# Optimization experiments

Measured on AMD Instinct MI355X. Metric: run time of the kernel, lower is better.

The kernel has to match this reference:

```python
import jax, jax.numpy as jnp
import numpy as np

N_VERTEX = 16384
D_IN = 64
HIDDEN = 64
D_OUT = 8
N_REGIONS = 64


def setup_inputs() -> dict:
    key = jax.random.key(0)
    ks = jax.random.split(key, 16)
    h = jax.random.normal(ks[0], (N_VERTEX, D_IN), dtype=jnp.float32)
    norm_adj = jax.random.uniform(ks[1], (N_VERTEX, N_VERTEX), dtype=jnp.float32) / N_VERTEX
    region_index = jax.random.randint(ks[2], (N_VERTEX,), 0, N_REGIONS, dtype=jnp.int32)
    s = 1.0 / np.sqrt(D_IN)
    W1 = jax.random.normal(ks[3], (D_IN, HIDDEN), dtype=jnp.float32) * s
    L1 = jax.random.normal(ks[4], (D_IN, HIDDEN), dtype=jnp.float32) * s
    rw1 = jax.random.normal(ks[5], (N_REGIONS, HIDDEN), dtype=jnp.float32) * 0.1 + 1.0
    rb1 = jax.random.normal(ks[6], (N_REGIONS, HIDDEN), dtype=jnp.float32) * 0.1
    sh = 1.0 / np.sqrt(HIDDEN)
    W2 = jax.random.normal(ks[7], (HIDDEN, HIDDEN), dtype=jnp.float32) * sh
    L2 = jax.random.normal(ks[8], (HIDDEN, HIDDEN), dtype=jnp.float32) * sh
    rw2 = jax.random.normal(ks[9], (N_REGIONS, HIDDEN), dtype=jnp.float32) * 0.1 + 1.0
    rb2 = jax.random.normal(ks[10], (N_REGIONS, HIDDEN), dtype=jnp.float32) * 0.1
    Wout = jax.random.normal(ks[11], (D_OUT, HIDDEN), dtype=jnp.float32) * sh
    bout = jax.random.normal(ks[12], (D_OUT,), dtype=jnp.float32) * 0.1
    return dict(h=h, norm_adj=norm_adj, region_index=region_index,
                W1=W1, L1=L1, rw1=rw1, rb1=rb1,
                W2=W2, L2=L2, rw2=rw2, rb2=rb2,
                Wout=Wout, bout=bout)


def _reg_conv(h, norm_adj, region_index, W, L, reg_w, reg_b):
    # ra = h @ W ; rb = norm_adj @ (h @ L)   [N, d_out]
    z = h @ W + norm_adj @ (h @ L)
    # per-vertex region gather of affine params (the irregular-access hot path)
    return z * reg_w[region_index] + reg_b[region_index]


def reference(h, norm_adj, region_index, W1, L1, rw1, rb1, W2, L2, rw2, rb2, Wout, bout):
    x = jax.nn.relu(_reg_conv(h, norm_adj, region_index, W1, L1, rw1, rb1))
    x = jax.nn.relu(_reg_conv(x, norm_adj, region_index, W2, L2, rw2, rb2))
    return x @ Wout.T + bout  # [N, d_out]
```

## Files before the change

kernel.cpp:

```cpp
#include <hip/hip_runtime.h>
#include <stdint.h>

#define NV 16384
#define DH 64
#define BTS (NV + 64)
#define BTQS (NV + 64)
#define BK 256
#define LDST 264
#define LDST8 272
#define NCH 32
#define SCUP 16384.0f
#define SCDN 6.103515625e-05f

typedef __attribute__((ext_vector_type(4))) float f32x4;
typedef __attribute__((ext_vector_type(8))) short s16x8;

static __device__ __forceinline__ unsigned short f2bf(float f) {
  union { float f; unsigned u; } x; x.f = f;
  unsigned r = x.u + 0x7fffu + ((x.u >> 16) & 1u);
  return (unsigned short)(r >> 16);
}

static __device__ __forceinline__ s16x8 cvt8(f32x4 a, f32x4 b) {
  s16x8 r;
  r[0] = (short)f2bf(a[0]); r[1] = (short)f2bf(a[1]);
  r[2] = (short)f2bf(a[2]); r[3] = (short)f2bf(a[3]);
  r[4] = (short)f2bf(b[0]); r[5] = (short)f2bf(b[1]);
  r[6] = (short)f2bf(b[2]); r[7] = (short)f2bf(b[3]);
  return r;
}

__global__ __launch_bounds__(256) void k_prep(
    const float* __restrict__ h, const float* __restrict__ W1,
    const float* __restrict__ L1, float* __restrict__ Z,
    unsigned short* __restrict__ Bt) {
  __shared__ float Ws[4096], Ls[4096], hs[16 * 64];
  int tid = threadIdx.x;
  for (int i = tid; i < 4096; i += 256) { Ws[i] = W1[i]; Ls[i] = L1[i]; }
  int r = tid >> 6, c = tid & 63;
  int i0 = blockIdx.x << 4;
  #pragma unroll
  for (int m = 0; m < 4; ++m)
    hs[(r + 4 * m) * 64 + c] = h[(size_t)(i0 + r + 4 * m) * 64 + c];
  __syncthreads();
  float a1[4] = {0.f, 0.f, 0.f, 0.f};
  float a2[4] = {0.f, 0.f, 0.f, 0.f};
  #pragma unroll 8
  for (int k = 0; k < 64; ++k) {
    float wv = Ws[k * 64 + c];
    float lv = Ls[k * 64 + c];
    #pragma unroll
    for (int m = 0; m < 4; ++m) {
      float hv = hs[(r + 4 * m) * 64 + k];
      a1[m] += hv * wv;
      a2[m] += hv * lv;
    }
  }
  #pragma unroll
  for (int m = 0; m < 4; ++m) {
    int i = i0 + r + 4 * m;
    Z[(size_t)i * 64 + c] = a1[m];
    Bt[(size_t)c * BTS + i] = f2bf(a2[m]);
  }
}

__global__ __launch_bounds__(256, 2) void k_adj(
    const float* __restrict__ adj, const unsigned short* __restrict__ Bt,
    float* __restrict__ P, unsigned char* __restrict__ adj8) {
  __shared__ __align__(16) unsigned short Blds[2 * 64 * LDST];
  const int tid = threadIdx.x;
  const int lane = tid & 63;
  const int w = tid >> 6;
  const int l15 = lane & 15;
  const int kgrp = lane >> 4;
  const int xb = blockIdx.x;
  const int yb = blockIdx.y;
  const int row = (xb << 6) + (w << 4) + l15;
  const int kbase = yb << 13;

  const int srow = tid >> 4;
  const int sc16 = tid & 15;
  const unsigned short* sbase = Bt + (size_t)srow * BTS + kbase + sc16 * 8;
  unsigned short* lbase = Blds + srow * LDST + sc16 * 8;

  const float* ap = adj + (size_t)row * NV + kbase + kgrp * 8;
  unsigned char* a8w = adj8 +
      ((((size_t)xb * 2 + yb) * 4 + w) * 256) * 512 + (size_t)lane * 8;
  const int bofs0 = (l15 +  0) * LDST + kgrp * 8;
  const int bofs1 = (l15 + 16) * LDST + kgrp * 8;
  const int bofs2 = (l15 + 32) * LDST + kgrp * 8;
  const int bofs3 = (l15 + 48) * LDST + kgrp * 8;

  f32x4 sr0, sr1, sr2, sr3, sr4, sr5, sr6, sr7;
#define STAGE_LOAD(KC)                                                   \
  { const unsigned short* s_ = sbase + (KC);                             \
    sr0 = *(const f32x4*)(s_);                                           \
    sr1 = *(const f32x4*)(s_ + 128);                                     \
    sr2 = *(const f32x4*)(s_ + (size_t)16 * BTS);                        \
    sr3 = *(const f32x4*)(s_ + (size_t)16 * BTS + 128);                  \
    sr4 = *(const f32x4*)(s_ + (size_t)32 * BTS);                        \
    sr5 = *(const f32x4*)(s_ + (size_t)32 * BTS + 128);                  \
    sr6 = *(const f32x4*)(s_ + (size_t)48 * BTS);                        \
    sr7 = *(const f32x4*)(s_ + (size_t)48 * BTS + 128); }
#define STAGE_WRITE(BUF)                                                 \
  { unsigned short* d_ = lbase + (BUF) * (64 * LDST);                    \
    *(f32x4*)(d_) = sr0;                                                 \
    *(f32x4*)(d_ + 128) = sr1;                                           \
    *(f32x4*)(d_ + 16 * LDST) = sr2;                                     \
    *(f32x4*)(d_ + 16 * LDST + 128) = sr3;                               \
    *(f32x4*)(d_ + 32 * LDST) = sr4;                                     \
    *(f32x4*)(d_ + 32 * LDST + 128) = sr5;                               \
    *(f32x4*)(d_ + 48 * LDST) = sr6;                                     \
    *(f32x4*)(d_ + 48 * LDST + 128) = sr7; }

  f32x4 aj0a, aj0b, aj1a, aj1b, aj2a, aj2b, aj3a, aj3b;

  STAGE_LOAD(0);
  aj0a = *(const f32x4*)(ap +   0); aj0b = *(const f32x4*)(ap +   4);
  aj1a = *(const f32x4*)(ap +  32); aj1b = *(const f32x4*)(ap +  36);
  aj2a = *(const f32x4*)(ap +  64); aj2b = *(const f32x4*)(ap +  68);
  aj3a = *(const f32x4*)(ap +  96); aj3b = *(const f32x4*)(ap + 100);
  STAGE_WRITE(0);
  __syncthreads();

  f32x4 acc0 = {0.f, 0.f, 0.f, 0.f};
  f32x4 acc1 = {0.f, 0.f, 0.f, 0.f};
  f32x4 acc2 = {0.f, 0.f, 0.f, 0.f};
  f32x4 acc3 = {0.f, 0.f, 0.f, 0.f};

#define ITER(II, AJA, AJB)                                               \
  {                                                                      \
    s16x8 af = cvt8(AJA, AJB);                                           \
    unsigned pk0 = __builtin_amdgcn_cvt_pk_fp8_f32(AJA[0] * SCUP, AJA[1] * SCUP, 0, false); \
    pk0 = __builtin_amdgcn_cvt_pk_fp8_f32(AJA[2] * SCUP, AJA[3] * SCUP, pk0, true);         \
    unsigned pk1 = __builtin_amdgcn_cvt_pk_fp8_f32(AJB[0] * SCUP, AJB[1] * SCUP, 0, false); \
    pk1 = __builtin_amdgcn_cvt_pk_fp8_f32(AJB[2] * SCUP, AJB[3] * SCUP, pk1, true);         \
    *(unsigned long long*)(a8w + (size_t)((t << 3) + (II)) * 512) =      \
        (unsigned long long)pk0 | ((unsigned long long)pk1 << 32);       \
    int ci = ((t << 3) + (II) + 4) & 255;                                \
    AJA = *(const f32x4*)(ap + (size_t)ci * 32);                         \
    AJB = *(const f32x4*)(ap + (size_t)ci * 32 + 4);                     \
    s16x8 cb0 = *(const s16x8*)(bb + bofs0 + (II) * 32);                 \
    s16x8 cb1 = *(const s16x8*)(bb + bofs1 + (II) * 32);                 \
    s16x8 cb2 = *(const s16x8*)(bb + bofs2 + (II) * 32);                 \
    s16x8 cb3 = *(const s16x8*)(bb + bofs3 + (II) * 32);                 \
    acc0 = __builtin_amdgcn_mfma_f32_16x16x32_bf16(af, cb0, acc0, 0, 0, 0); \
    acc1 = __builtin_amdgcn_mfma_f32_16x16x32_bf16(af, cb1, acc1, 0, 0, 0); \
    acc2 = __builtin_amdgcn_mfma_f32_16x16x32_bf16(af, cb2, acc2, 0, 0, 0); \
    acc3 = __builtin_amdgcn_mfma_f32_16x16x32_bf16(af, cb3, acc3, 0, 0, 0); \
  }

  for (int t = 0; t < NCH; ++t) {
    const unsigned short* bb = Blds + (t & 1) * (64 * LDST);
    if (t + 1 < NCH) STAGE_LOAD((t + 1) * BK);
    ITER(0, aj0a, aj0b)
    ITER(1, aj1a, aj1b)
    ITER(2, aj2a, aj2b)
    ITER(3, aj3a, aj3b)
    ITER(4, aj0a, aj0b)
    ITER(5, aj1a, aj1b)
    ITER(6, aj2a, aj2b)
    ITER(7, aj3a, aj3b)
    if (t + 1 < NCH) STAGE_WRITE((t + 1) & 1);
    __syncthreads();
  }

  int zr = (xb << 6) + (w << 4) + (kgrp << 2);
  float* pp = P + (size_t)yb * NV * 64 + (size_t)zr * 64 + l15;
  #pragma unroll
  for (int r = 0; r < 4; ++r) {
    pp[(size_t)r * 64 +  0] = acc0[r];
    pp[(size_t)r * 64 + 16] = acc1[r];
    pp[(size_t)r * 64 + 32] = acc2[r];
    pp[(size_t)r * 64 + 48] = acc3[r];
  }
#undef STAGE_LOAD
#undef STAGE_WRITE
#undef ITER
}

__global__ __launch_bounds__(256, 2) void k_adj8(
    const unsigned char* __restrict__ adj8, const unsigned char* __restrict__ Btq,
    float* __restrict__ P) {
  __shared__ __align__(16) unsigned char Blds[2 * 64 * LDST8];
  const int tid = threadIdx.x;
  const int lane = tid & 63;
  const int w = tid >> 6;
  const int l15 = lane & 15;
  const int kgrp = lane >> 4;
  const int xb = blockIdx.x;
  const int yb = blockIdx.y;
  const int kbase = yb << 13;

  const int srow = tid >> 4;
  const int sc16 = tid & 15;
  const unsigned char* sbase = Btq + (size_t)srow * BTQS + kbase + sc16 * 16;
  unsigned char* lbase = Blds + srow * LDST8 + sc16 * 16;

  const unsigned char* ap8 = adj8 +
      ((((size_t)xb * 2 + yb) * 4 + w) * 256) * 512 + (size_t)lane * 8;
  const int bofs0 = (l15 +  0) * LDST8 + kgrp * 8;
  const int bofs1 = (l15 + 16) * LDST8 + kgrp * 8;
  const int bofs2 = (l15 + 32) * LDST8 + kgrp * 8;
  const int bofs3 = (l15 + 48) * LDST8 + kgrp * 8;

  f32x4 sr0, sr1, sr2, sr3;
#define STAGE_LOAD8(KC)                                                  \
  { const unsigned char* s_ = sbase + (KC);                              \
    sr0 = *(const f32x4*)(s_);                                           \
    sr1 = *(const f32x4*)(s_ + (size_t)16 * BTQS);                       \
    sr2 = *(const f32x4*)(s_ + (size_t)32 * BTQS);                       \
    sr3 = *(const f32x4*)(s_ + (size_t)48 * BTQS); }
#define STAGE_WRITE8(BUF)                                                \
  { unsigned char* d_ = lbase + (BUF) * (64 * LDST8);                    \
    *(f32x4*)(d_) = sr0;                                                 \
    *(f32x4*)(d_ + 16 * LDST8) = sr1;                                    \
    *(f32x4*)(d_ + 32 * LDST8) = sr2;                                    \
    *(f32x4*)(d_ + 48 * LDST8) = sr3; }

  unsigned long long aj0, aj1, aj2, aj3;

  STAGE_LOAD8(0);
  aj0 = *(const unsigned long long*)(ap8 +    0);
  aj1 = *(const unsigned long long*)(ap8 +  512);
  aj2 = *(const unsigned long long*)(ap8 + 1024);
  aj3 = *(const unsigned long long*)(ap8 + 1536);
  STAGE_WRITE8(0);
  __syncthreads();

  f32x4 acc0 = {0.f, 0.f, 0.f, 0.f};
  f32x4 acc1 = {0.f, 0.f, 0.f, 0.f};
  f32x4 acc2 = {0.f, 0.f, 0.f, 0.f};
  f32x4 acc3 = {0.f, 0.f, 0.f, 0.f};

#define ITER8(II, AJ)                                                    \
  {                                                                      \
    long long a_ = (long long)AJ;                                        \
    int ci = ((t << 3) + (II) + 4) & 255;                                \
    AJ = *(const unsigned long long*)(ap8 + (size_t)ci * 512);           \
    long long b0 = *(const long long*)(bb + bofs0 + (II) * 32);          \
    long long b1 = *(const long long*)(bb + bofs1 + (II) * 32);          \
    long long b2 = *(const long long*)(bb + bofs2 + (II) * 32);          \
    long long b3 = *(const long long*)(bb + bofs3 + (II) * 32);          \
    acc0 = __builtin_amdgcn_mfma_f32_16x16x32_fp8_fp8(a_, b0, acc0, 0, 0, 0); \
    acc1 = __builtin_amdgcn_mfma_f32_16x16x32_fp8_fp8(a_, b1, acc1, 0, 0, 0); \
    acc2 = __builtin_amdgcn_mfma_f32_16x16x32_fp8_fp8(a_, b2, acc2, 0, 0, 0); \
    acc3 = __builtin_amdgcn_mfma_f32_16x16x32_fp8_fp8(a_, b3, acc3, 0, 0, 0); \
  }

  for (int t = 0; t < NCH; ++t) {
    const unsigned char* bb = Blds + (t & 1) * (64 * LDST8);
    if (t + 1 < NCH) STAGE_LOAD8((t + 1) * BK);
    ITER8(0, aj0)
    ITER8(1, aj1)
    ITER8(2, aj2)
    ITER8(3, aj3)
    ITER8(4, aj0)
    ITER8(5, aj1)
    ITER8(6, aj2)
    ITER8(7, aj3)
    if (t + 1 < NCH) STAGE_WRITE8((t + 1) & 1);
    __syncthreads();
  }

  int zr = (xb << 6) + (w << 4) + (kgrp << 2);
  float* pp = P + (size_t)yb * NV * 64 + (size_t)zr * 64 + l15;
  #pragma unroll
  for (int r = 0; r < 4; ++r) {
    pp[(size_t)r * 64 +  0] = acc0[r] * SCDN;
    pp[(size_t)r * 64 + 16] = acc1[r] * SCDN;
    pp[(size_t)r * 64 + 32] = acc2[r] * SCDN;
    pp[(size_t)r * 64 + 48] = acc3[r] * SCDN;
  }
#undef STAGE_LOAD8
#undef STAGE_WRITE8
#undef ITER8
}

__global__ __launch_bounds__(256) void k_mid(
    float* __restrict__ Z, const float* __restrict__ P,
    const int* __restrict__ reg,
    const float* __restrict__ rw1, const float* __restrict__ rb1,
    const float* __restrict__ W2, const float* __restrict__ L2,
    unsigned char* __restrict__ Btq) {
  __shared__ float Ws[4096], Ls[4096], xs[16 * 64];
  int tid = threadIdx.x;
  for (int i = tid; i < 4096; i += 256) { Ws[i] = W2[i]; Ls[i] = L2[i]; }
  int r = tid >> 6, c = tid & 63;
  int i0 = blockIdx.x << 4;
  #pragma unroll
  for (int m = 0; m < 4; ++m) {
    int i = i0 + r + 4 * m;
    int ri = reg[i];
    size_t o = (size_t)i * 64 + c;
    float z = Z[o] + P[o] + P[(size_t)NV * 64 + o];
    float x = z * rw1[ri * 64 + c] + rb1[ri * 64 + c];
    xs[(r + 4 * m) * 64 + c] = fmaxf(x, 0.f);
  }
  __syncthreads();
  float a1[4] = {0.f, 0.f, 0.f, 0.f};
  float a2[4] = {0.f, 0.f, 0.f, 0.f};
  #pragma unroll 8
  for (int k = 0; k < 64; ++k) {
    float wv = Ws[k * 64 + c];
    float lv = Ls[k * 64 + c];
    #pragma unroll
    for (int m = 0; m < 4; ++m) {
      float xv = xs[(r + 4 * m) * 64 + k];
      a1[m] += xv * wv;
      a2[m] += xv * lv;
    }
  }
  #pragma unroll
  for (int m = 0; m < 4; ++m) {
    int i = i0 + r + 4 * m;
    Z[(size_t)i * 64 + c] = a1[m];
    unsigned q = __builtin_amdgcn_cvt_pk_fp8_f32(a2[m], 0.0f, 0, false);
    Btq[(size_t)c * BTQS + i] = (unsigned char)(q & 0xff);
  }
}

__global__ __launch_bounds__(256) void k_out(
    const float* __restrict__ Z, const float* __restrict__ P,
    const int* __restrict__ reg,
    const float* __restrict__ rw2, const float* __restrict__ rb2,
    const float* __restrict__ Wout, const float* __restrict__ bout,
    float* __restrict__ out) {
  __shared__ float xs[16 * 64];
  int tid = threadIdx.x;
  int r = tid >> 6, c = tid & 63;
  int i0 = blockIdx.x << 4;
  #pragma unroll
  for (int m = 0; m < 4; ++m) {
    int i = i0 + r + 4 * m;
    int ri = reg[i];
    size_t o = (size_t)i * 64 + c;
    float z = Z[o] + P[o] + P[(size_t)NV * 64 + o];
    float x = z * rw2[ri * 64 + c] + rb2[ri * 64 + c];
    xs[(r + 4 * m) * 64 + c] = fmaxf(x, 0.f);
  }
  __syncthreads();
  if (c < 8) {
    #pragma unroll
    for (int m = 0; m < 4; ++m) {
      int i = i0 + r + 4 * m;
      float a = bout[c];
      #pragma unroll 8
      for (int k = 0; k < 64; ++k) a += xs[(r + 4 * m) * 64 + k] * Wout[c * 64 + k];
      out[(size_t)i * 8 + c] = a;
    }
  }
}

extern "C" void kernel_launch(void* const* d_in, const int* in_sizes, int n_in,
                              void* d_out, int out_size, void* d_ws, size_t ws_size,
                              hipStream_t stream) {
  const float* h    = (const float*)d_in[0];
  const float* adj  = (const float*)d_in[1];
  const int*   reg  = (const int*)d_in[2];
  const float* W1   = (const float*)d_in[3];
  const float* L1   = (const float*)d_in[4];
  const float* rw1  = (const float*)d_in[5];
  const float* rb1  = (const float*)d_in[6];
  const float* W2   = (const float*)d_in[7];
  const float* L2   = (const float*)d_in[8];
  const float* rw2  = (const float*)d_in[9];
  const float* rb2  = (const float*)d_in[10];
  const float* Wout = (const float*)d_in[11];
  const float* bout = (const float*)d_in[12];
  float* out = (float*)d_out;

  char* ws = (char*)d_ws;
  float* Z            = (float*)(ws);
  unsigned short* Bt  = (unsigned short*)(ws + ((size_t)4  << 20));
  float* P            = (float*)(ws + ((size_t)8  << 20));
  unsigned char* Btq  = (unsigned char*)(ws + ((size_t)16 << 20));
  unsigned char* adj8 = (unsigned char*)(ws + ((size_t)20 << 20));

  k_prep<<<NV / 16, 256, 0, stream>>>(h, W1, L1, Z, Bt);
  k_adj<<<dim3(NV / 64, 2), 256, 0, stream>>>(adj, Bt, P, adj8);
  k_mid<<<NV / 16, 256, 0, stream>>>(Z, P, reg, rw1, rb1, W2, L2, Btq);
  k_adj8<<<dim3(NV / 64, 2), 256, 0, stream>>>(adj8, Btq, P);
  k_out<<<NV / 16, 256, 0, stream>>>(Z, P, reg, rw2, rb2, Wout, bout, out);
}
```

Baseline: 405.6 us.

## Use FP8 MFMA for first adjacency pass and split K four ways

The first adjacency GEMM now quantizes both the adjacency rows and the h@L1 operand to FP8 and uses the FP8 16x16x32 MFMA, replacing the bf16 path. This removes the bf16 conversion work and halves the shared-memory staging. The K dimension is also split into four partial sums instead of two, doubling the grid and raising occupancy hints to 4 blocks per CU, with the consumers now summing four partial planes. This trades accuracy for speed, since the first layer's operand also becomes FP8, and it adds extra partial-sum memory traffic.

```diff
diff --git a/kernel.cpp b/kernel.cpp
--- a/kernel.cpp
+++ b/kernel.cpp
@@ -2,38 +2,19 @@
 #include <stdint.h>
 
 #define NV 16384
-#define DH 64
-#define BTS (NV + 64)
 #define BTQS (NV + 64)
 #define BK 256
-#define LDST 264
 #define LDST8 272
-#define NCH 32
+#define NCH 16
 #define SCUP 16384.0f
 #define SCDN 6.103515625e-05f
 
 typedef __attribute__((ext_vector_type(4))) float f32x4;
-typedef __attribute__((ext_vector_type(8))) short s16x8;
-
-static __device__ __forceinline__ unsigned short f2bf(float f) {
-  union { float f; unsigned u; } x; x.f = f;
-  unsigned r = x.u + 0x7fffu + ((x.u >> 16) & 1u);
-  return (unsigned short)(r >> 16);
-}
-
-static __device__ __forceinline__ s16x8 cvt8(f32x4 a, f32x4 b) {
-  s16x8 r;
-  r[0] = (short)f2bf(a[0]); r[1] = (short)f2bf(a[1]);
-  r[2] = (short)f2bf(a[2]); r[3] = (short)f2bf(a[3]);
-  r[4] = (short)f2bf(b[0]); r[5] = (short)f2bf(b[1]);
-  r[6] = (short)f2bf(b[2]); r[7] = (short)f2bf(b[3]);
-  return r;
-}
 
 __global__ __launch_bounds__(256) void k_prep(
     const float* __restrict__ h, const float* __restrict__ W1,
     const float* __restrict__ L1, float* __restrict__ Z,
-    unsigned short* __restrict__ Bt) {
+    unsigned char* __restrict__ Btq1) {
   __shared__ float Ws[4096], Ls[4096], hs[16 * 64];
   int tid = threadIdx.x;
   for (int i = tid; i < 4096; i += 256) { Ws[i] = W1[i]; Ls[i] = L1[i]; }
@@ -60,14 +41,15 @@
   for (int m = 0; m < 4; ++m) {
     int i = i0 + r + 4 * m;
     Z[(size_t)i * 64 + c] = a1[m];
-    Bt[(size_t)c * BTS + i] = f2bf(a2[m]);
-  }
-}
-
-__global__ __launch_bounds__(256, 2) void k_adj(
-    const float* __restrict__ adj, const unsigned short* __restrict__ Bt,
+    unsigned q = __builtin_amdgcn_cvt_pk_fp8_f32(a2[m], 0.0f, 0, false);
+    Btq1[(size_t)c * BTQS + i] = (unsigned char)(q & 0xff);
+  }
+}
+
+__global__ __launch_bounds__(256, 4) void k_adj1(
+    const float* __restrict__ adj, const unsigned char* __restrict__ Btq,
     float* __restrict__ P, unsigned char* __restrict__ adj8) {
-  __shared__ __align__(16) unsigned short Blds[2 * 64 * LDST];
+  __shared__ __align__(16) unsigned char Blds[2 * 64 * LDST8];
   const int tid = threadIdx.x;
   const int lane = tid & 63;
   const int w = tid >> 6;
@@ -76,129 +58,16 @@
   const int xb = blockIdx.x;
   const int yb = blockIdx.y;
   const int row = (xb << 6) + (w << 4) + l15;
-  const int kbase = yb << 13;
-
-  const int srow = tid >> 4;
-  const int sc16 = tid & 15;
-  const unsigned short* sbase = Bt + (size_t)srow * BTS + kbase + sc16 * 8;
-  unsigned short* lbase = Blds + srow * LDST + sc16 * 8;
-
-  const float* ap = adj + (size_t)row * NV + kbase + kgrp * 8;
-  unsigned char* a8w = adj8 +
-      ((((size_t)xb * 2 + yb) * 4 + w) * 256) * 512 + (size_t)lane * 8;
-  const int bofs0 = (l15 +  0) * LDST + kgrp * 8;
-  const int bofs1 = (l15 + 16) * LDST + kgrp * 8;
-  const int bofs2 = (l15 + 32) * LDST + kgrp * 8;
-  const int bofs3 = (l15 + 48) * LDST + kgrp * 8;
-
-  f32x4 sr0, sr1, sr2, sr3, sr4, sr5, sr6, sr7;
-#define STAGE_LOAD(KC)                                                   \
-  { const unsigned short* s_ = sbase + (KC);                             \
-    sr0 = *(const f32x4*)(s_);                                           \
-    sr1 = *(const f32x4*)(s_ + 128);                                     \
-    sr2 = *(const f32x4*)(s_ + (size_t)16 * BTS);                        \
-    sr3 = *(const f32x4*)(s_ + (size_t)16 * BTS + 128);                  \
-    sr4 = *(const f32x4*)(s_ + (size_t)32 * BTS);                        \
-    sr5 = *(const f32x4*)(s_ + (size_t)32 * BTS + 128);                  \
-    sr6 = *(const f32x4*)(s_ + (size_t)48 * BTS);                        \
-    sr7 = *(const f32x4*)(s_ + (size_t)48 * BTS + 128); }
-#define STAGE_WRITE(BUF)                                                 \
-  { unsigned short* d_ = lbase + (BUF) * (64 * LDST);                    \
-    *(f32x4*)(d_) = sr0;                                                 \
-    *(f32x4*)(d_ + 128) = sr1;                                           \
-    *(f32x4*)(d_ + 16 * LDST) = sr2;                                     \
-    *(f32x4*)(d_ + 16 * LDST + 128) = sr3;                               \
-    *(f32x4*)(d_ + 32 * LDST) = sr4;                                     \
-    *(f32x4*)(d_ + 32 * LDST + 128) = sr5;                               \
-    *(f32x4*)(d_ + 48 * LDST) = sr6;                                     \
-    *(f32x4*)(d_ + 48 * LDST + 128) = sr7; }
-
-  f32x4 aj0a, aj0b, aj1a, aj1b, aj2a, aj2b, aj3a, aj3b;
-
-  STAGE_LOAD(0);
-  aj0a = *(const f32x4*)(ap +   0); aj0b = *(const f32x4*)(ap +   4);
-  aj1a = *(const f32x4*)(ap +  32); aj1b = *(const f32x4*)(ap +  36);
-  aj2a = *(const f32x4*)(ap +  64); aj2b = *(const f32x4*)(ap +  68);
-  aj3a = *(const f32x4*)(ap +  96); aj3b = *(const f32x4*)(ap + 100);
-  STAGE_WRITE(0);
-  __syncthreads();
-
-  f32x4 acc0 = {0.f, 0.f, 0.f, 0.f};
-  f32x4 acc1 = {0.f, 0.f, 0.f, 0.f};
-  f32x4 acc2 = {0.f, 0.f, 0.f, 0.f};
-  f32x4 acc3 = {0.f, 0.f, 0.f, 0.f};
-
-#define ITER(II, AJA, AJB)                                               \
-  {                                                                      \
-    s16x8 af = cvt8(AJA, AJB);                                           \
-    unsigned pk0 = __builtin_amdgcn_cvt_pk_fp8_f32(AJA[0] * SCUP, AJA[1] * SCUP, 0, false); \
-    pk0 = __builtin_amdgcn_cvt_pk_fp8_f32(AJA[2] * SCUP, AJA[3] * SCUP, pk0, true);         \
-    unsigned pk1 = __builtin_amdgcn_cvt_pk_fp8_f32(AJB[0] * SCUP, AJB[1] * SCUP, 0, false); \
-    pk1 = __builtin_amdgcn_cvt_pk_fp8_f32(AJB[2] * SCUP, AJB[3] * SCUP, pk1, true);         \
-    *(unsigned long long*)(a8w + (size_t)((t << 3) + (II)) * 512) =      \
-        (unsigned long long)pk0 | ((unsigned long long)pk1 << 32);       \
-    int ci = ((t << 3) + (II) + 4) & 255;                                \
-    AJA = *(const f32x4*)(ap + (size_t)ci * 32);                         \
-    AJB = *(const f32x4*)(ap + (size_t)ci * 32 + 4);                     \
-    s16x8 cb0 = *(const s16x8*)(bb + bofs0 + (II) * 32);                 \
-    s16x8 cb1 = *(const s16x8*)(bb + bofs1 + (II) * 32);                 \
-    s16x8 cb2 = *(const s16x8*)(bb + bofs2 + (II) * 32);                 \
-    s16x8 cb3 = *(const s16x8*)(bb + bofs3 + (II) * 32);                 \
-    acc0 = __builtin_amdgcn_mfma_f32_16x16x32_bf16(af, cb0, acc0, 0, 0, 0); \
-    acc1 = __builtin_amdgcn_mfma_f32_16x16x32_bf16(af, cb1, acc1, 0, 0, 0); \
-    acc2 = __builtin_amdgcn_mfma_f32_16x16x32_bf16(af, cb2, acc2, 0, 0, 0); \
-    acc3 = __builtin_amdgcn_mfma_f32_16x16x32_bf16(af, cb3, acc3, 0, 0, 0); \
-  }
-
-  for (int t = 0; t < NCH; ++t) {
-    const unsigned short* bb = Blds + (t & 1) * (64 * LDST);
-    if (t + 1 < NCH) STAGE_LOAD((t + 1) * BK);
-    ITER(0, aj0a, aj0b)
-    ITER(1, aj1a, aj1b)
-    ITER(2, aj2a, aj2b)
-    ITER(3, aj3a, aj3b)
-    ITER(4, aj0a, aj0b)
-    ITER(5, aj1a, aj1b)
-    ITER(6, aj2a, aj2b)
-    ITER(7, aj3a, aj3b)
-    if (t + 1 < NCH) STAGE_WRITE((t + 1) & 1);
-    __syncthreads();
-  }
-
-  int zr = (xb << 6) + (w << 4) + (kgrp << 2);
-  float* pp = P + (size_t)yb * NV * 64 + (size_t)zr * 64 + l15;
-  #pragma unroll
-  for (int r = 0; r < 4; ++r) {
-    pp[(size_t)r * 64 +  0] = acc0[r];
-    pp[(size_t)r * 64 + 16] = acc1[r];
-    pp[(size_t)r * 64 + 32] = acc2[r];
-    pp[(size_t)r * 64 + 48] = acc3[r];
-  }
-#undef STAGE_LOAD
-#undef STAGE_WRITE
-#undef ITER
-}
-
-__global__ __launch_bounds__(256, 2) void k_adj8(
-    const unsigned char* __restrict__ adj8, const unsigned char* __restrict__ Btq,
-    float* __restrict__ P) {
-  __shared__ __align__(16) unsigned char Blds[2 * 64 * LDST8];
-  const int tid = threadIdx.x;
-  const int lane = tid & 63;
-  const int w = tid >> 6;
-  const int l15 = lane & 15;
-  const int kgrp = lane >> 4;
-  const int xb = blockIdx.x;
-  const int yb = blockIdx.y;
-  const int kbase = yb << 13;
+  const int kbase = yb << 12;
 
   const int srow = tid >> 4;
   const int sc16 = tid & 15;
   const unsigned char* sbase = Btq + (size_t)srow * BTQS + kbase + sc16 * 16;
   unsigned char* lbase = Blds + srow * LDST8 + sc16 * 16;
 
-  const unsigned char* ap8 = adj8 +
-      ((((size_t)xb * 2 + yb) * 4 + w) * 256) * 512 + (size_t)lane * 8;
+  const float* ap = adj + (size_t)row * NV + kbase + kgrp * 8;
+  unsigned char* a8w = adj8 +
+      ((((size_t)xb * 4 + yb) * 4 + w) * 128) * 512 + (size_t)lane * 8;
   const int bofs0 = (l15 +  0) * LDST8 + kgrp * 8;
   const int bofs1 = (l15 + 16) * LDST8 + kgrp * 8;
   const int bofs2 = (l15 + 32) * LDST8 + kgrp * 8;
@@ -218,6 +87,97 @@
     *(f32x4*)(d_ + 32 * LDST8) = sr2;                                    \
     *(f32x4*)(d_ + 48 * LDST8) = sr3; }
 
+  f32x4 aj0a, aj0b, aj1a, aj1b, aj2a, aj2b, aj3a, aj3b;
+
+  STAGE_LOAD8(0);
+  aj0a = *(const f32x4*)(ap +   0); aj0b = *(const f32x4*)(ap +   4);
+  aj1a = *(const f32x4*)(ap +  32); aj1b = *(const f32x4*)(ap +  36);
+  aj2a = *(const f32x4*)(ap +  64); aj2b = *(const f32x4*)(ap +  68);
+  aj3a = *(const f32x4*)(ap +  96); aj3b = *(const f32x4*)(ap + 100);
+  STAGE_WRITE8(0);
+  __syncthreads();
+
+  f32x4 acc0 = {0.f, 0.f, 0.f, 0.f};
+  f32x4 acc1 = {0.f, 0.f, 0.f, 0.f};
+  f32x4 acc2 = {0.f, 0.f, 0.f, 0.f};
+  f32x4 acc3 = {0.f, 0.f, 0.f, 0.f};
+
+#define ITER1(II, AJA, AJB)                                              \
+  {                                                                      \
+    unsigned pk0 = __builtin_amdgcn_cvt_pk_fp8_f32(AJA[0] * SCUP, AJA[1] * SCUP, 0, false); \
+    pk0 = __builtin_amdgcn_cvt_pk_fp8_f32(AJA[2] * SCUP, AJA[3] * SCUP, pk0, true);         \
+    unsigned pk1 = __builtin_amdgcn_cvt_pk_fp8_f32(AJB[0] * SCUP, AJB[1] * SCUP, 0, false); \
+    pk1 = __builtin_amdgcn_cvt_pk_fp8_f32(AJB[2] * SCUP, AJB[3] * SCUP, pk1, true);         \
+    unsigned long long av = (unsigned long long)pk0 | ((unsigned long long)pk1 << 32); \
+    *(unsigned long long*)(a8w + (size_t)((t << 3) + (II)) * 512) = av;  \
+    long long a_ = (long long)av;                                        \
+    int ci = ((t << 3) + (II) + 4) & 127;                                \
+    AJA = *(const f32x4*)(ap + (size_t)ci * 32);                         \
+    AJB = *(const f32x4*)(ap + (size_t)ci * 32 + 4);                     \
+    long long b0 = *(const long long*)(bb + bofs0 + (II) * 32);          \
+    long long b1 = *(const long long*)(bb + bofs1 + (II) * 32);          \
+    long long b2 = *(const long long*)(bb + bofs2 + (II) * 32);          \
+    long long b3 = *(const long long*)(bb + bofs3 + (II) * 32);          \
+    acc0 = __builtin_amdgcn_mfma_f32_16x16x32_fp8_fp8(a_, b0, acc0, 0, 0, 0); \
+    acc1 = __builtin_amdgcn_mfma_f32_16x16x32_fp8_fp8(a_, b1, acc1, 0, 0, 0); \
+    acc2 = __builtin_amdgcn_mfma_f32_16x16x32_fp8_fp8(a_, b2, acc2, 0, 0, 0); \
+    acc3 = __builtin_amdgcn_mfma_f32_16x16x32_fp8_fp8(a_, b3, acc3, 0, 0, 0); \
+  }
+
+  for (int t = 0; t < NCH; ++t) {
+    const unsigned char* bb = Blds + (t & 1) * (64 * LDST8);
+    if (t + 1 < NCH) STAGE_LOAD8((t + 1) * BK);
+    ITER1(0, aj0a, aj0b)
+    ITER1(1, aj1a, aj1b)
+    ITER1(2, aj2a, aj2b)
+    ITER1(3, aj3a, aj3b)
+    ITER1(4, aj0a, aj0b)
+    ITER1(5, aj1a, aj1b)
+    ITER1(6, aj2a, aj2b)
+    ITER1(7, aj3a, aj3b)
+    if (t + 1 < NCH) STAGE_WRITE8((t + 1) & 1);
+    __syncthreads();
+  }
+
+  int zr = (xb << 6) + (w << 4) + (kgrp << 2);
+  float* pp = P + (size_t)yb * NV * 64 + (size_t)zr * 64 + l15;
+  #pragma unroll
+  for (int r = 0; r < 4; ++r) {
+    pp[(size_t)r * 64 +  0] = acc0[r] * SCDN;
+    pp[(size_t)r * 64 + 16] = acc1[r] * SCDN;
+    pp[(size_t)r * 64 + 32] = acc2[r] * SCDN;
+    pp[(size_t)r * 64 + 48] = acc3[r] * SCDN;
+  }
+#undef ITER1
+}
+
+__global__ __launch_bounds__(256, 4) void k_adj8(
+    const unsigned char* __restrict__ adj8, const unsigned char* __restrict__ Btq,
+    float* __restrict__ P) {
+  __shared__ __align__(16) unsigned char Blds[2 * 64 * LDST8];
+  const int tid = threadIdx.x;
+  const int lane = tid & 63;
+  const int w = tid >> 6;
+  const int l15 = lane & 15;
+  const int kgrp = lane >> 4;
+  const int xb = blockIdx.x;
+  const int yb = blockIdx.y;
+  const int kbase = yb << 12;
+
+  const int srow = tid >> 4;
+  const int sc16 = tid & 15;
+  const unsigned char* sbase = Btq + (size_t)srow * BTQS + kbase + sc16 * 16;
+  unsigned char* lbase = Blds + srow * LDST8 + sc16 * 16;
+
+  const unsigned char* ap8 = adj8 +
+      ((((size_t)xb * 4 + yb) * 4 + w) * 128) * 512 + (size_t)lane * 8;
+  const int bofs0 = (l15 +  0) * LDST8 + kgrp * 8;
+  const int bofs1 = (l15 + 16) * LDST8 + kgrp * 8;
+  const int bofs2 = (l15 + 32) * LDST8 + kgrp * 8;
+  const int bofs3 = (l15 + 48) * LDST8 + kgrp * 8;
+
+  f32x4 sr0, sr1, sr2, sr3;
+
   unsigned long long aj0, aj1, aj2, aj3;
 
   STAGE_LOAD8(0);
@@ -236,7 +196,7 @@
 #define ITER8(II, AJ)                                                    \
   {                                                                      \
     long long a_ = (long long)AJ;                                        \
-    int ci = ((t << 3) + (II) + 4) & 255;                                \
+    int ci = ((t << 3) + (II) + 4) & 127;                                \
     AJ = *(const unsigned long long*)(ap8 + (size_t)ci * 512);           \
     long long b0 = *(const long long*)(bb + bofs0 + (II) * 32);          \
     long long b1 = *(const long long*)(bb + bofs1 + (II) * 32);          \
@@ -272,9 +232,9 @@
     pp[(size_t)r * 64 + 32] = acc2[r] * SCDN;
     pp[(size_t)r * 64 + 48] = acc3[r] * SCDN;
   }
+#undef ITER8
 #undef STAGE_LOAD8
 #undef STAGE_WRITE8
-#undef ITER8
 }
 
 __global__ __launch_bounds__(256) void k_mid(
@@ -282,7 +242,7 @@
     const int* __restrict__ reg,
     const float* __restrict__ rw1, const float* __restrict__ rb1,
     const float* __restrict__ W2, const float* __restrict__ L2,
-    unsigned char* __restrict__ Btq) {
+    unsigned char* __restrict__ Btq2) {
   __shared__ float Ws[4096], Ls[4096], xs[16 * 64];
   int tid = threadIdx.x;
   for (int i = tid; i < 4096; i += 256) { Ws[i] = W2[i]; Ls[i] = L2[i]; }
@@ -293,7 +253,8 @@
     int i = i0 + r + 4 * m;
     int ri = reg[i];
     size_t o = (size_t)i * 64 + c;
-    float z = Z[o] + P[o] + P[(size_t)NV * 64 + o];
+    float z = Z[o] + P[o] + P[(size_t)NV * 64 + o] +
+              P[(size_t)2 * NV * 64 + o] + P[(size_t)3 * NV * 64 + o];
     float x = z * rw1[ri * 64 + c] + rb1[ri * 64 + c];
     xs[(r + 4 * m) * 64 + c] = fmaxf(x, 0.f);
   }
@@ -316,7 +277,7 @@
     int i = i0 + r + 4 * m;
     Z[(size_t)i * 64 + c] = a1[m];
     unsigned q = __builtin_amdgcn_cvt_pk_fp8_f32(a2[m], 0.0f, 0, false);
-    Btq[(size_t)c * BTQS + i] = (unsigned char)(q & 0xff);
+    Btq2[(size_t)c * BTQS + i] = (unsigned char)(q & 0xff);
   }
 }
 
@@ -335,7 +296,8 @@
     int i = i0 + r + 4 * m;
     int ri = reg[i];
     size_t o = (size_t)i * 64 + c;
-    float z = Z[o] + P[o] + P[(size_t)NV * 64 + o];
+    float z = Z[o] + P[o] + P[(size_t)NV * 64 + o] +
+              P[(size_t)2 * NV * 64 + o] + P[(size_t)3 * NV * 64 + o];
     float x = z * rw2[ri * 64 + c] + rb2[ri * 64 + c];
     xs[(r + 4 * m) * 64 + c] = fmaxf(x, 0.f);
   }
@@ -372,14 +334,14 @@
 
   char* ws = (char*)d_ws;
   float* Z            = (float*)(ws);
-  unsigned short* Bt  = (unsigned short*)(ws + ((size_t)4  << 20));
+  unsigned char* Btq1 = (unsigned char*)(ws + ((size_t)4  << 20));
   float* P            = (float*)(ws + ((size_t)8  << 20));
-  unsigned char* Btq  = (unsigned char*)(ws + ((size_t)16 << 20));
-  unsigned char* adj8 = (unsigned char*)(ws + ((size_t)20 << 20));
-
-  k_prep<<<NV / 16, 256, 0, stream>>>(h, W1, L1, Z, Bt);
-  k_adj<<<dim3(NV / 64, 2), 256, 0, stream>>>(adj, Bt, P, adj8);
-  k_mid<<<NV / 16, 256, 0, stream>>>(Z, P, reg, rw1, rb1, W2, L2, Btq);
-  k_adj8<<<dim3(NV / 64, 2), 256, 0, stream>>>(adj8, Btq, P);
+  unsigned char* Btq2 = (unsigned char*)(ws + ((size_t)24 << 20));
+  unsigned char* adj8 = (unsigned char*)(ws + ((size_t)28 << 20));
+
+  k_prep<<<NV / 16, 256, 0, stream>>>(h, W1, L1, Z, Btq1);
+  k_adj1<<<dim3(NV / 64, 4), 256, 0, stream>>>(adj, Btq1, P, adj8);
+  k_mid<<<NV / 16, 256, 0, stream>>>(Z, P, reg, rw1, rb1, W2, L2, Btq2);
+  k_adj8<<<dim3(NV / 64, 4), 256, 0, stream>>>(adj8, Btq2, P);
   k_out<<<NV / 16, 256, 0, stream>>>(Z, P, reg, rw2, rb2, Wout, bout, out);
 }
```

Measured after the change: 395.5 us. -2.5%, faster.
